# Performance work log

Measured on AMD Instinct MI355X. Metric: run time of the kernel, lower is better.

## Reference

```python
import jax, jax.numpy as jnp
import numpy as np
import math

B, S, D, H = 2, 2048, 1024, 16
DK = D // H


def setup_inputs() -> dict:
    key = jax.random.key(0)
    ks = jax.random.split(key, 12)
    s = 1.0 / math.sqrt(D)
    inp = {
        "q": jax.random.normal(ks[0], (B, S, D), jnp.float32),
        "k": jax.random.normal(ks[1], (B, S, D), jnp.float32),
        "v": jax.random.normal(ks[2], (B, S, D), jnp.float32),
        "mask": jnp.broadcast_to(jnp.tril(jnp.ones((S, S), jnp.int32))[None, None], (B, 1, S, S)),
        "Wq": jax.random.normal(ks[3], (D, D), jnp.float32) * s,
        "bq": jnp.zeros((D,), jnp.float32),
        "Wk": jax.random.normal(ks[4], (D, D), jnp.float32) * s,
        "bk": jnp.zeros((D,), jnp.float32),
        "Wv": jax.random.normal(ks[5], (D, D), jnp.float32) * s,
        "bv": jnp.zeros((D,), jnp.float32),
        "Wo": jax.random.normal(ks[6], (D, D), jnp.float32) * s,
        "bo": jnp.zeros((D,), jnp.float32),
    }
    return inp


def reference(q, k, v, mask, Wq, bq, Wk, bk, Wv, bv, Wo, bo):
    b = q.shape[0]
    # project and split heads -> [b, h, s, d_k]
    def heads(x, W, bias):
        y = x @ W.T + bias
        return y.reshape(b, -1, H, DK).transpose(0, 2, 1, 3)
    qh = heads(q, Wq, bq)
    kh = heads(k, Wk, bk)
    vh = heads(v, Wv, bv)
    scores = jnp.einsum("bhqd,bhkd->bhqk", qh, kh) / math.sqrt(DK)
    scores = jnp.where(mask == 0, jnp.float32(-1e9), scores)
    weights = jax.nn.softmax(scores, axis=-1)  # dropout p=0 -> identity
    out = jnp.einsum("bhqk,bhkd->bhqd", weights, vh)
    out = out.transpose(0, 2, 1, 3).reshape(b, -1, H * DK)
    return out @ Wo.T + bo
```

## Files before the change

### kernel.cpp

```cpp
#include <hip/hip_runtime.h>

#define B_ 2
#define S_ 2048
#define D_ 1024
#define H_ 16
#define DK_ 64
#define M_ 4096

typedef unsigned short u16;
typedef __bf16 bf16x8 __attribute__((ext_vector_type(8)));
typedef float floatx4 __attribute__((ext_vector_type(4)));

#if __has_builtin(__builtin_amdgcn_exp2f)
#define EXP2F(x) __builtin_amdgcn_exp2f(x)
#else
#define EXP2F(x) exp2f(x)
#endif

__device__ __forceinline__ u16 f2bf(float f) {
  unsigned u = __float_as_uint(f);
  u += 0x7fffu + ((u >> 16) & 1u);
  return (u16)(u >> 16);
}

__device__ __forceinline__ void stage16(const void* g, void* l) {
  __builtin_amdgcn_global_load_lds(
      (const __attribute__((address_space(1))) unsigned int*)g,
      (__attribute__((address_space(3))) unsigned int*)l, 16, 0, 0);
}

__global__ __launch_bounds__(256) void cvt_all_kernel(
    const float* __restrict__ q, const float* __restrict__ k, const float* __restrict__ v,
    const float* __restrict__ wq, const float* __restrict__ wk,
    const float* __restrict__ wv, const float* __restrict__ wo,
    u16* dq, u16* dk, u16* dv, u16* dwq, u16* dwk, u16* dwv, u16* dwo) {
  const float* s; u16* d; size_t base;
  const int bx = blockIdx.x;
  if (bx < 6144) {
    const int t0 = bx >> 11;
    base = (size_t)(bx & 2047) * 2048;
    s = t0 == 0 ? q : t0 == 1 ? k : v;
    d = t0 == 0 ? dq : t0 == 1 ? dk : dv;
  } else {
    const int t0 = (bx - 6144) >> 9;
    base = (size_t)((bx - 6144) & 511) * 2048;
    s = t0 == 0 ? wq : t0 == 1 ? wk : t0 == 2 ? wv : wo;
    d = t0 == 0 ? dwq : t0 == 1 ? dwk : t0 == 2 ? dwv : dwo;
  }
  const size_t i = base + (size_t)threadIdx.x * 8;
  const float4 f0 = *reinterpret_cast<const float4*>(s + i);
  const float4 f1 = *reinterpret_cast<const float4*>(s + i + 4);
  union { u16 h[8]; uint4 u; } cv;
  cv.h[0] = f2bf(f0.x); cv.h[1] = f2bf(f0.y); cv.h[2] = f2bf(f0.z); cv.h[3] = f2bf(f0.w);
  cv.h[4] = f2bf(f1.x); cv.h[5] = f2bf(f1.y); cv.h[6] = f2bf(f1.z); cv.h[7] = f2bf(f1.w);
  *reinterpret_cast<uint4*>(d + i) = cv.u;
}

template <int BN>
__device__ __forceinline__ void gemm_body(
    const u16* __restrict__ A, const u16* __restrict__ W,
    const float* __restrict__ bias, void* __restrict__ outp,
    int mode, float scale) {
  constexpr int NT = BN / 32;
  constexpr int NB = BN / 32;
  __shared__ __align__(16) u16 As[128 * 64];
  __shared__ __align__(16) u16 Bs[BN * 64];

  const int t = threadIdx.x;
  const int lane = t & 63, w = t >> 6;
  const int quad = lane >> 4, l16 = lane & 15;
  const int wm = w >> 1, wn = w & 1;
  const int m0 = blockIdx.y * 128, n0 = blockIdx.x * BN;

  const u16 *gA[4], *gB[NB]; u16 *lA[4], *lB[NB];
#pragma unroll
  for (int i = 0; i < 4; i++) {
    const int ch = (i * 4 + w) * 64 + lane;
    const int row = ch >> 3, c = ch & 7, cs = c ^ (row & 7);
    gA[i] = A + (size_t)(m0 + row) * 1024 + cs * 8;
    lA[i] = As + ((i * 4 + w) * 64) * 8;
  }
#pragma unroll
  for (int i = 0; i < NB; i++) {
    const int ch = (i * 4 + w) * 64 + lane;
    const int row = ch >> 3, c = ch & 7, cs = c ^ (row & 7);
    gB[i] = W + (size_t)(n0 + row) * 1024 + cs * 8;
    lB[i] = Bs + ((i * 4 + w) * 64) * 8;
  }

  floatx4 acc[4][NT] = {};

  for (int k0 = 0; k0 < 1024; k0 += 64) {
    __syncthreads();
#pragma unroll
    for (int i = 0; i < 4; i++) stage16(gA[i] + k0, lA[i]);
#pragma unroll
    for (int i = 0; i < NB; i++) stage16(gB[i] + k0, lB[i]);
    __syncthreads();
#pragma unroll
    for (int kk = 0; kk < 2; kk++) {
      bf16x8 af[4], bf[NT];
      const int sw = (kk * 4 + quad) ^ (l16 & 7);
#pragma unroll
      for (int mt = 0; mt < 4; mt++) {
        const int row = wm * 64 + mt * 16 + l16;
        af[mt] = *reinterpret_cast<const bf16x8*>(&As[(row * 8 + sw) * 8]);
      }
#pragma unroll
      for (int nt = 0; nt < NT; nt++) {
        const int row = wn * (NT * 16) + nt * 16 + l16;
        bf[nt] = *reinterpret_cast<const bf16x8*>(&Bs[(row * 8 + sw) * 8]);
      }
#pragma unroll
      for (int mt = 0; mt < 4; mt++)
#pragma unroll
        for (int nt = 0; nt < NT; nt++)
          acc[mt][nt] = __builtin_amdgcn_mfma_f32_16x16x32_bf16(af[mt], bf[nt], acc[mt][nt], 0, 0, 0);
    }
  }

#pragma unroll
  for (int mt = 0; mt < 4; mt++) {
    const int mbase = m0 + wm * 64 + mt * 16 + quad * 4;
    const int bb = mbase >> 11, s0v = mbase & 2047;
#pragma unroll
    for (int nt = 0; nt < NT; nt++) {
      const int n = n0 + wn * (NT * 16) + nt * 16 + l16;
      const float bvv = bias[n];
      if (mode == 0) {
        u16* Y = (u16*)outp;
        const int h = n >> 6, dk = n & 63;
#pragma unroll
        for (int r = 0; r < 4; r++)
          Y[(((size_t)(bb * H_ + h)) * S_ + (s0v + r)) * DK_ + dk] =
              f2bf((acc[mt][nt][r] + bvv) * scale);
      } else if (mode == 2) {
        u16* Y = (u16*)outp;
        const int h = n >> 6, dk = n & 63;
        union { u16 h4[4]; uint2 u; } pk2;
#pragma unroll
        for (int r = 0; r < 4; r++) pk2.h4[r] = f2bf(acc[mt][nt][r] + bvv);
        *reinterpret_cast<uint2*>(
            &Y[(((size_t)(bb * H_ + h)) * DK_ + dk) * S_ + s0v]) = pk2.u;
      } else {
        float* Y = (float*)outp;
#pragma unroll
        for (int r = 0; r < 4; r++)
          Y[(size_t)(mbase + r) * 1024 + n] = acc[mt][nt][r] + bvv;
      }
    }
  }
}

__global__ __launch_bounds__(256) void qkv_gemm_kernel(
    const u16* qa, const u16* ka, const u16* va,
    const u16* wq, const u16* wk, const u16* wv,
    const float* bq, const float* bk, const float* bv,
    u16* Qh, u16* Kh, u16* VhT) {
  const int g = blockIdx.z;
  const u16* A = g == 0 ? qa : g == 1 ? ka : va;
  const u16* W = g == 0 ? wq : g == 1 ? wk : wv;
  const float* bias = g == 0 ? bq : g == 1 ? bk : bv;
  void* out = g == 0 ? (void*)Qh : g == 1 ? (void*)Kh : (void*)VhT;
  gemm_body<128>(A, W, bias, out, g == 2 ? 2 : 0, g == 0 ? 0.18033688011112f : 1.0f);
}

__global__ __launch_bounds__(256) void o_gemm_kernel(
    const u16* ctx, const u16* wo, const float* bo, float* out) {
  gemm_body<64>(ctx, wo, bo, out, 3, 1.0f);
}

__global__ __launch_bounds__(256) void attn_kernel(
    const u16* __restrict__ Qh, const u16* __restrict__ Kh,
    const u16* __restrict__ VhT, u16* __restrict__ Ctx) {
  __shared__ __align__(16) u16 Kt[64 * 64];
  __shared__ __align__(16) u16 Vt[64 * 64];
  __shared__ __align__(16) u16 Ps[128 * 72];

  const int t = threadIdx.x;
  const int lane = t & 63, w = t >> 6;
  const int quad = lane >> 4, l16 = lane & 15;

  const int qi = 15 - (blockIdx.x >> 5);
  const int bh = blockIdx.x & 31;
  const int qb = qi * 128;
  const u16* Qp = Qh + (size_t)bh * S_ * DK_;
  const u16* Kp = Kh + (size_t)bh * S_ * DK_;
  const u16* Vp = VhT + (size_t)bh * DK_ * S_;

  bf16x8 bq[2][2];
#pragma unroll
  for (int g = 0; g < 2; g++)
#pragma unroll
    for (int kk = 0; kk < 2; kk++)
      bq[g][kk] = *reinterpret_cast<const bf16x8*>(
          &Qp[(size_t)(qb + w * 32 + g * 16 + l16) * DK_ + kk * 32 + quad * 8]);

  const u16 *gK[2], *gV[2]; u16 *lK[2], *lV[2];
#pragma unroll
  for (int i = 0; i < 2; i++) {
    const int ch = (i * 4 + w) * 64 + lane;
    const int row = ch >> 3, c = ch & 7, cs = c ^ (row & 7);
    gK[i] = Kp + (size_t)row * DK_ + cs * 8;
    gV[i] = Vp + (size_t)row * S_ + cs * 8;
    lK[i] = Kt + ((i * 4 + w) * 64) * 8;
    lV[i] = Vt + ((i * 4 + w) * 64) * 8;
  }

  float l_run[2] = {0.f, 0.f};
  floatx4 o[2][4] = {};
  const int ntile = (qb + 128) >> 6;

  for (int it = 0; it < ntile; it++) {
    const int j0 = it * 64;
    __syncthreads();
#pragma unroll
    for (int i = 0; i < 2; i++) {
      stage16(gK[i] + (size_t)j0 * DK_, lK[i]);
      stage16(gV[i] + j0, lV[i]);
    }
    __syncthreads();

    floatx4 sc[2][4] = {};
#pragma unroll
    for (int mt = 0; mt < 4; mt++) {
      const int row = mt * 16 + l16;
#pragma unroll
      for (int kk = 0; kk < 2; kk++) {
        const bf16x8 ak = *reinterpret_cast<const bf16x8*>(
            &Kt[(row * 8 + ((kk * 4 + quad) ^ (l16 & 7))) * 8]);
        sc[0][mt] = __builtin_amdgcn_mfma_f32_16x16x32_bf16(ak, bq[0][kk], sc[0][mt], 0, 0, 0);
        sc[1][mt] = __builtin_amdgcn_mfma_f32_16x16x32_bf16(ak, bq[1][kk], sc[1][mt], 0, 0, 0);
      }
    }

    const bool maskT = (it >= ntile - 2);
#pragma unroll
    for (int g = 0; g < 2; g++) {
      const int qg = qb + w * 32 + g * 16 + l16;
      float psum = 0.f;
#pragma unroll
      for (int mt = 0; mt < 4; mt++) {
        float p[4];
#pragma unroll
        for (int r = 0; r < 4; r++) {
          float vsc = sc[g][mt][r];
          if (maskT && (j0 + mt * 16 + quad * 4 + r > qg)) vsc = -1e30f;
          p[r] = EXP2F(vsc);
          psum += p[r];
        }
        uint2 pu;
        pu.x = (__float_as_uint(p[1]) & 0xffff0000u) | (__float_as_uint(p[0]) >> 16);
        pu.y = (__float_as_uint(p[3]) & 0xffff0000u) | (__float_as_uint(p[2]) >> 16);
        *reinterpret_cast<uint2*>(
            &Ps[(w * 32 + g * 16 + l16) * 72 + mt * 16 + quad * 4]) = pu;
      }
      psum += __shfl_xor(psum, 16);
      psum += __shfl_xor(psum, 32);
      l_run[g] += psum;
    }

#pragma unroll
    for (int kk = 0; kk < 2; kk++) {
      const bf16x8 ap0 = *reinterpret_cast<const bf16x8*>(
          &Ps[(w * 32 + l16) * 72 + kk * 32 + quad * 8]);
      const bf16x8 ap1 = *reinterpret_cast<const bf16x8*>(
          &Ps[(w * 32 + 16 + l16) * 72 + kk * 32 + quad * 8]);
#pragma unroll
      for (int nt = 0; nt < 4; nt++) {
        const bf16x8 bv = *reinterpret_cast<const bf16x8*>(
            &Vt[((nt * 16 + l16) * 8 + ((kk * 4 + quad) ^ (l16 & 7))) * 8]);
        o[0][nt] = __builtin_amdgcn_mfma_f32_16x16x32_bf16(ap0, bv, o[0][nt], 0, 0, 0);
        o[1][nt] = __builtin_amdgcn_mfma_f32_16x16x32_bf16(ap1, bv, o[1][nt], 0, 0, 0);
      }
    }
  }

  const int bb = bh >> 4, hh = bh & 15;
#pragma unroll
  for (int g = 0; g < 2; g++)
#pragma unroll
    for (int r = 0; r < 4; r++) {
      const float lr = __shfl(l_run[g], quad * 4 + r);
      const float inv = 1.0f / lr;
      const int srow = qb + w * 32 + g * 16 + quad * 4 + r;
      u16* cp = Ctx + ((size_t)bb * S_ + srow) * D_ + hh * DK_;
#pragma unroll
      for (int nt = 0; nt < 4; nt++)
        cp[nt * 16 + l16] = f2bf(o[g][nt][r] * inv);
    }
}

extern "C" void kernel_launch(void* const* d_in, const int* in_sizes, int n_in,
                              void* d_out, int out_size, void* d_ws, size_t ws_size,
                              hipStream_t stream) {
  const float* q  = (const float*)d_in[0];
  const float* k  = (const float*)d_in[1];
  const float* v  = (const float*)d_in[2];
  const float* Wq = (const float*)d_in[4];
  const float* bq = (const float*)d_in[5];
  const float* Wk = (const float*)d_in[6];
  const float* bk = (const float*)d_in[7];
  const float* Wv = (const float*)d_in[8];
  const float* bv = (const float*)d_in[9];
  const float* Wo = (const float*)d_in[10];
  const float* bo = (const float*)d_in[11];

  const size_t nW = (size_t)D_ * D_;
  const size_t nA = (size_t)M_ * D_;
  u16* wqb = (u16*)d_ws;
  u16* wkb = wqb + nW;
  u16* wvb = wkb + nW;
  u16* wob = wvb + nW;
  u16* qb_ = wob + nW;
  u16* kb_ = qb_ + nA;
  u16* vb_ = kb_ + nA;
  u16* Qh  = vb_ + nA;
  u16* Kh  = Qh + nA;
  u16* VhT = Kh + nA;
  u16* Ctx = qb_;

  cvt_all_kernel<<<dim3(8192), 256, 0, stream>>>(q, k, v, Wq, Wk, Wv, Wo,
                                                 qb_, kb_, vb_, wqb, wkb, wvb, wob);

  qkv_gemm_kernel<<<dim3(D_ / 128, M_ / 128, 3), 256, 0, stream>>>(
      qb_, kb_, vb_, wqb, wkb, wvb, bq, bk, bv, Qh, Kh, VhT);

  attn_kernel<<<dim3(B_ * H_ * (S_ / 128)), 256, 0, stream>>>(Qh, Kh, VhT, Ctx);

  o_gemm_kernel<<<dim3(D_ / 64, M_ / 128), 256, 0, stream>>>(Ctx, wob, bo, (float*)d_out);
}
```

Before: 257.6 us.

## Halve attention query tile with balanced scheduling and split-K output projection

The attention kernel now gives each block a 64-row query tile instead of 128, doubling the grid and ordering tiles in a zigzag so causal work is balanced across waves. This also trims masked work to only the diagonal tile. The output projection is split along K into two halves that accumulate into a zeroed output with float atomics, doubling its grid. The costs are an extra memset, atomic traffic, less K/V reuse per block, and non-deterministic summation order.

```diff
diff --git a/kernel.cpp b/kernel.cpp
--- a/kernel.cpp
+++ b/kernel.cpp
@@ -60,7 +60,7 @@
 __device__ __forceinline__ void gemm_body(
     const u16* __restrict__ A, const u16* __restrict__ W,
     const float* __restrict__ bias, void* __restrict__ outp,
-    int mode, float scale) {
+    int mode, float scale, int kbeg, int kend) {
   constexpr int NT = BN / 32;
   constexpr int NB = BN / 32;
   __shared__ __align__(16) u16 As[128 * 64];
@@ -90,7 +90,7 @@
 
   floatx4 acc[4][NT] = {};
 
-  for (int k0 = 0; k0 < 1024; k0 += 64) {
+  for (int k0 = kbeg; k0 < kend; k0 += 64) {
     __syncthreads();
 #pragma unroll
     for (int i = 0; i < 4; i++) stage16(gA[i] + k0, lA[i]);
@@ -126,7 +126,7 @@
 #pragma unroll
     for (int nt = 0; nt < NT; nt++) {
       const int n = n0 + wn * (NT * 16) + nt * 16 + l16;
-      const float bvv = bias[n];
+      const float bvv = (mode == 4 && kbeg != 0) ? 0.f : bias[n];
       if (mode == 0) {
         u16* Y = (u16*)outp;
         const int h = n >> 6, dk = n & 63;
@@ -146,7 +146,7 @@
         float* Y = (float*)outp;
 #pragma unroll
         for (int r = 0; r < 4; r++)
-          Y[(size_t)(mbase + r) * 1024 + n] = acc[mt][nt][r] + bvv;
+          unsafeAtomicAdd(&Y[(size_t)(mbase + r) * 1024 + n], acc[mt][nt][r] + bvv);
       }
     }
   }
@@ -162,12 +162,13 @@
   const u16* W = g == 0 ? wq : g == 1 ? wk : wv;
   const float* bias = g == 0 ? bq : g == 1 ? bk : bv;
   void* out = g == 0 ? (void*)Qh : g == 1 ? (void*)Kh : (void*)VhT;
-  gemm_body<128>(A, W, bias, out, g == 2 ? 2 : 0, g == 0 ? 0.18033688011112f : 1.0f);
+  gemm_body<128>(A, W, bias, out, g == 2 ? 2 : 0,
+                 g == 0 ? 0.18033688011112f : 1.0f, 0, 1024);
 }
 
 __global__ __launch_bounds__(256) void o_gemm_kernel(
     const u16* ctx, const u16* wo, const float* bo, float* out) {
-  gemm_body<64>(ctx, wo, bo, out, 3, 1.0f);
+  gemm_body<64>(ctx, wo, bo, out, 4, 1.0f, blockIdx.z * 512, blockIdx.z * 512 + 512);
 }
 
 __global__ __launch_bounds__(256) void attn_kernel(
@@ -175,53 +176,55 @@
     const u16* __restrict__ VhT, u16* __restrict__ Ctx) {
   __shared__ __align__(16) u16 Kt[64 * 64];
   __shared__ __align__(16) u16 Vt[64 * 64];
-  __shared__ __align__(16) u16 Ps[128 * 72];
+  __shared__ __align__(16) u16 Ps[64 * 72];
 
   const int t = threadIdx.x;
   const int lane = t & 63, w = t >> 6;
   const int quad = lane >> 4, l16 = lane & 15;
 
-  const int qi = 15 - (blockIdx.x >> 5);
   const int bh = blockIdx.x & 31;
-  const int qb = qi * 128;
+  const int i = blockIdx.x >> 5;
+  const int j = i >> 3, r0 = i & 7;
+  const int u = (j == 0) ? 31 - r0 : (j == 1) ? r0 : (j == 2) ? 23 - r0 : 8 + r0;
+  const int qb = u * 64;
+  const int ntile = u + 1;
+
   const u16* Qp = Qh + (size_t)bh * S_ * DK_;
   const u16* Kp = Kh + (size_t)bh * S_ * DK_;
   const u16* Vp = VhT + (size_t)bh * DK_ * S_;
 
-  bf16x8 bq[2][2];
-#pragma unroll
-  for (int g = 0; g < 2; g++)
-#pragma unroll
-    for (int kk = 0; kk < 2; kk++)
-      bq[g][kk] = *reinterpret_cast<const bf16x8*>(
-          &Qp[(size_t)(qb + w * 32 + g * 16 + l16) * DK_ + kk * 32 + quad * 8]);
+  bf16x8 bq[2];
+#pragma unroll
+  for (int kk = 0; kk < 2; kk++)
+    bq[kk] = *reinterpret_cast<const bf16x8*>(
+        &Qp[(size_t)(qb + w * 16 + l16) * DK_ + kk * 32 + quad * 8]);
 
   const u16 *gK[2], *gV[2]; u16 *lK[2], *lV[2];
 #pragma unroll
-  for (int i = 0; i < 2; i++) {
-    const int ch = (i * 4 + w) * 64 + lane;
+  for (int i2 = 0; i2 < 2; i2++) {
+    const int ch = (i2 * 4 + w) * 64 + lane;
     const int row = ch >> 3, c = ch & 7, cs = c ^ (row & 7);
-    gK[i] = Kp + (size_t)row * DK_ + cs * 8;
-    gV[i] = Vp + (size_t)row * S_ + cs * 8;
-    lK[i] = Kt + ((i * 4 + w) * 64) * 8;
-    lV[i] = Vt + ((i * 4 + w) * 64) * 8;
-  }
-
-  float l_run[2] = {0.f, 0.f};
-  floatx4 o[2][4] = {};
-  const int ntile = (qb + 128) >> 6;
+    gK[i2] = Kp + (size_t)row * DK_ + cs * 8;
+    gV[i2] = Vp + (size_t)row * S_ + cs * 8;
+    lK[i2] = Kt + ((i2 * 4 + w) * 64) * 8;
+    lV[i2] = Vt + ((i2 * 4 + w) * 64) * 8;
+  }
+
+  float l_run = 0.f;
+  floatx4 o[4] = {};
+  const int qg = qb + w * 16 + l16;
 
   for (int it = 0; it < ntile; it++) {
     const int j0 = it * 64;
     __syncthreads();
 #pragma unroll
-    for (int i = 0; i < 2; i++) {
-      stage16(gK[i] + (size_t)j0 * DK_, lK[i]);
-      stage16(gV[i] + j0, lV[i]);
+    for (int i2 = 0; i2 < 2; i2++) {
+      stage16(gK[i2] + (size_t)j0 * DK_, lK[i2]);
+      stage16(gV[i2] + j0, lV[i2]);
     }
     __syncthreads();
 
-    floatx4 sc[2][4] = {};
+    floatx4 sc[4] = {};
 #pragma unroll
     for (int mt = 0; mt < 4; mt++) {
       const int row = mt * 16 + l16;
@@ -229,66 +232,55 @@
       for (int kk = 0; kk < 2; kk++) {
         const bf16x8 ak = *reinterpret_cast<const bf16x8*>(
             &Kt[(row * 8 + ((kk * 4 + quad) ^ (l16 & 7))) * 8]);
-        sc[0][mt] = __builtin_amdgcn_mfma_f32_16x16x32_bf16(ak, bq[0][kk], sc[0][mt], 0, 0, 0);
-        sc[1][mt] = __builtin_amdgcn_mfma_f32_16x16x32_bf16(ak, bq[1][kk], sc[1][mt], 0, 0, 0);
-      }
-    }
-
-    const bool maskT = (it >= ntile - 2);
-#pragma unroll
-    for (int g = 0; g < 2; g++) {
-      const int qg = qb + w * 32 + g * 16 + l16;
-      float psum = 0.f;
-#pragma unroll
-      for (int mt = 0; mt < 4; mt++) {
-        float p[4];
-#pragma unroll
-        for (int r = 0; r < 4; r++) {
-          float vsc = sc[g][mt][r];
-          if (maskT && (j0 + mt * 16 + quad * 4 + r > qg)) vsc = -1e30f;
-          p[r] = EXP2F(vsc);
-          psum += p[r];
-        }
-        uint2 pu;
-        pu.x = (__float_as_uint(p[1]) & 0xffff0000u) | (__float_as_uint(p[0]) >> 16);
-        pu.y = (__float_as_uint(p[3]) & 0xffff0000u) | (__float_as_uint(p[2]) >> 16);
-        *reinterpret_cast<uint2*>(
-            &Ps[(w * 32 + g * 16 + l16) * 72 + mt * 16 + quad * 4]) = pu;
-      }
-      psum += __shfl_xor(psum, 16);
-      psum += __shfl_xor(psum, 32);
-      l_run[g] += psum;
-    }
+        sc[mt] = __builtin_amdgcn_mfma_f32_16x16x32_bf16(ak, bq[kk], sc[mt], 0, 0, 0);
+      }
+    }
+
+    const bool maskT = (it == ntile - 1);
+    float psum = 0.f;
+#pragma unroll
+    for (int mt = 0; mt < 4; mt++) {
+      float p[4];
+#pragma unroll
+      for (int r = 0; r < 4; r++) {
+        float vsc = sc[mt][r];
+        if (maskT && (j0 + mt * 16 + quad * 4 + r > qg)) vsc = -1e30f;
+        p[r] = EXP2F(vsc);
+        psum += p[r];
+      }
+      uint2 pu;
+      pu.x = (__float_as_uint(p[1]) & 0xffff0000u) | (__float_as_uint(p[0]) >> 16);
+      pu.y = (__float_as_uint(p[3]) & 0xffff0000u) | (__float_as_uint(p[2]) >> 16);
+      *reinterpret_cast<uint2*>(&Ps[(w * 16 + l16) * 72 + mt * 16 + quad * 4]) = pu;
+    }
+    psum += __shfl_xor(psum, 16);
+    psum += __shfl_xor(psum, 32);
+    l_run += psum;
 
 #pragma unroll
     for (int kk = 0; kk < 2; kk++) {
-      const bf16x8 ap0 = *reinterpret_cast<const bf16x8*>(
-          &Ps[(w * 32 + l16) * 72 + kk * 32 + quad * 8]);
-      const bf16x8 ap1 = *reinterpret_cast<const bf16x8*>(
-          &Ps[(w * 32 + 16 + l16) * 72 + kk * 32 + quad * 8]);
+      const bf16x8 ap = *reinterpret_cast<const bf16x8*>(
+          &Ps[(w * 16 + l16) * 72 + kk * 32 + quad * 8]);
 #pragma unroll
       for (int nt = 0; nt < 4; nt++) {
         const bf16x8 bv = *reinterpret_cast<const bf16x8*>(
             &Vt[((nt * 16 + l16) * 8 + ((kk * 4 + quad) ^ (l16 & 7))) * 8]);
-        o[0][nt] = __builtin_amdgcn_mfma_f32_16x16x32_bf16(ap0, bv, o[0][nt], 0, 0, 0);
-        o[1][nt] = __builtin_amdgcn_mfma_f32_16x16x32_bf16(ap1, bv, o[1][nt], 0, 0, 0);
+        o[nt] = __builtin_amdgcn_mfma_f32_16x16x32_bf16(ap, bv, o[nt], 0, 0, 0);
       }
     }
   }
 
   const int bb = bh >> 4, hh = bh & 15;
 #pragma unroll
-  for (int g = 0; g < 2; g++)
-#pragma unroll
-    for (int r = 0; r < 4; r++) {
-      const float lr = __shfl(l_run[g], quad * 4 + r);
-      const float inv = 1.0f / lr;
-      const int srow = qb + w * 32 + g * 16 + quad * 4 + r;
-      u16* cp = Ctx + ((size_t)bb * S_ + srow) * D_ + hh * DK_;
-#pragma unroll
-      for (int nt = 0; nt < 4; nt++)
-        cp[nt * 16 + l16] = f2bf(o[g][nt][r] * inv);
-    }
+  for (int r = 0; r < 4; r++) {
+    const float lr = __shfl(l_run, quad * 4 + r);
+    const float inv = 1.0f / lr;
+    const int srow = qb + w * 16 + quad * 4 + r;
+    u16* cp = Ctx + ((size_t)bb * S_ + srow) * D_ + hh * DK_;
+#pragma unroll
+    for (int nt = 0; nt < 4; nt++)
+      cp[nt * 16 + l16] = f2bf(o[nt][r] * inv);
+  }
 }
 
 extern "C" void kernel_launch(void* const* d_in, const int* in_sizes, int n_in,
@@ -320,13 +312,15 @@
   u16* VhT = Kh + nA;
   u16* Ctx = qb_;
 
+  hipMemsetAsync(d_out, 0, (size_t)out_size * sizeof(float), stream);
+
   cvt_all_kernel<<<dim3(8192), 256, 0, stream>>>(q, k, v, Wq, Wk, Wv, Wo,
                                                  qb_, kb_, vb_, wqb, wkb, wvb, wob);
 
   qkv_gemm_kernel<<<dim3(D_ / 128, M_ / 128, 3), 256, 0, stream>>>(
       qb_, kb_, vb_, wqb, wkb, wvb, bq, bk, bv, Qh, Kh, VhT);
 
-  attn_kernel<<<dim3(B_ * H_ * (S_ / 128)), 256, 0, stream>>>(Qh, Kh, VhT, Ctx);
-
-  o_gemm_kernel<<<dim3(D_ / 64, M_ / 128), 256, 0, stream>>>(Ctx, wob, bo, (float*)d_out);
-}
+  attn_kernel<<<dim3(B_ * H_ * (S_ / 64)), 256, 0, stream>>>(Qh, Kh, VhT, Ctx);
+
+  o_gemm_kernel<<<dim3(D_ / 64, M_ / 128, 2), 256, 0, stream>>>(Ctx, wob, bo, (float*)d_out);
+}
```

Result: slower. 269.0 us (+4.4%).
